# Kernel tuning notes

Hardware: AMD Instinct MI355X
Metric: run time of the kernel (lower is better)

The kernel has to match this reference:

```python
import jax, jax.numpy as jnp
import numpy as np

DIM = 768
HEADS = 6
HD = DIM // HEADS
B, N = 8, 4096
EPS = 1e-12  # torch F.normalize default


def setup_inputs() -> dict:
    key = jax.random.key(0)
    k1, k2, k3, k4, k5 = jax.random.split(key, 5)
    x = jax.random.normal(k1, (B, N, DIM), dtype=jnp.float32)
    y = jax.random.normal(k2, (B, N, DIM), dtype=jnp.float32)
    W_qkv = jax.random.normal(k3, (DIM, 2 * DIM), dtype=jnp.float32) * (1.0 / np.sqrt(DIM))
    temperature = jnp.ones((HEADS, 1, 1), dtype=jnp.float32)
    W_proj = jax.random.normal(k4, (DIM, DIM), dtype=jnp.float32) * (1.0 / np.sqrt(DIM))
    b_proj = jax.random.normal(k5, (DIM,), dtype=jnp.float32) * 0.01
    return {"x": x, "y": y, "W_qkv": W_qkv, "temperature": temperature,
            "W_proj": W_proj, "b_proj": b_proj}


def _l2norm(t):
    # F.normalize(dim=-1): v / max(||v||, eps)
    n = jnp.sqrt(jnp.sum(t * t, axis=-1, keepdims=True))
    return t / jnp.maximum(n, EPS)


def reference(x, y, W_qkv, temperature, W_proj, b_proj):
    Bx, Nx, C = x.shape
    # qkv: [B,N,2C] -> [B,N,2,H,hd] -> q,k: [B,H,hd,N]
    qkv = (x @ W_qkv).reshape(Bx, Nx, 2, HEADS, HD)
    qkv = jnp.transpose(qkv, (2, 0, 3, 4, 1))  # [2,B,H,hd,N]
    q, k = qkv[0], qkv[1]
    # v: [B,H,hd,N]
    v = jnp.transpose(y.reshape(Bx, Nx, HEADS, HD), (0, 2, 3, 1))
    q = _l2norm(q)  # normalize over token dim N
    k = _l2norm(k)
    # channel-channel attention: [B,H,hd,hd]
    attn = jnp.einsum('bhcn,bhdn->bhcd', q, k) * temperature
    attn = jax.nn.softmax(attn, axis=-1)
    out = jnp.einsum('bhcd,bhdn->bhcn', attn, v)  # [B,H,hd,N]
    out = jnp.transpose(out, (0, 3, 1, 2)).reshape(Bx, Nx, C)
    return out @ W_proj + b_proj
```

## Files before the change

kernel.cpp:

```cpp
#include <hip/hip_runtime.h>
#include <hip/hip_bf16.h>

using bf16 = __hip_bfloat16;
typedef __attribute__((ext_vector_type(4))) float f32x4;
typedef __attribute__((ext_vector_type(8))) short bf16x8;

constexpr int Ntok   = 4096;
constexpr int Cdim   = 768;
constexpr int Hn     = 6;
constexpr int HD     = 128;
constexpr int QKcols = 1536;

#define AS1 __attribute__((address_space(1)))
#define AS3 __attribute__((address_space(3)))

__device__ inline void gload_lds16(const bf16* g, bf16* l) {
    __builtin_amdgcn_global_load_lds((const AS1 void*)g, (AS3 void*)l, 16, 0, 0);
}

__device__ inline int4 cvt8_f32_to_bf16(const float* p) {
    const float4 a0 = *reinterpret_cast<const float4*>(p);
    const float4 a1 = *reinterpret_cast<const float4*>(p + 4);
    union { int4 i; bf16 h[8]; } u;
    u.h[0] = __float2bfloat16(a0.x); u.h[1] = __float2bfloat16(a0.y);
    u.h[2] = __float2bfloat16(a0.z); u.h[3] = __float2bfloat16(a0.w);
    u.h[4] = __float2bfloat16(a1.x); u.h[5] = __float2bfloat16(a1.y);
    u.h[6] = __float2bfloat16(a1.z); u.h[7] = __float2bfloat16(a1.w);
    return u.i;
}

__global__ __launch_bounds__(256) void cvt_kernel(const float* __restrict__ in,
                                                  bf16* __restrict__ out) {
    const size_t i = ((size_t)blockIdx.x * 256 + threadIdx.x) * 8;
    *reinterpret_cast<int4*>(out + i) = cvt8_f32_to_bf16(in + i);
}

__global__ void transpose_kernel(const float* __restrict__ W, bf16* __restrict__ Wt,
                                 int K, int N) {
    __shared__ bf16 tile[32][33];
    const int n0 = blockIdx.x * 32, k0 = blockIdx.y * 32;
    const int tx = threadIdx.x, ty = threadIdx.y;
    for (int i = 0; i < 32; i += 8)
        tile[ty + i][tx] = __float2bfloat16(W[(size_t)(k0 + ty + i) * N + n0 + tx]);
    __syncthreads();
    for (int i = 0; i < 32; i += 8)
        Wt[(size_t)(n0 + ty + i) * K + k0 + tx] = tile[tx][ty + i];
}

template <bool C_F32, bool BIAS>
__global__ __launch_bounds__(256) void gemm_bt(const bf16* __restrict__ A,
                                               const bf16* __restrict__ Bt,
                                               const float* __restrict__ bias,
                                               void* __restrict__ Cv,
                                               int M, int N, int K) {
    __shared__ bf16 As[128 * 32];
    __shared__ bf16 Bs[128 * 32];

    const int m0   = blockIdx.y * 128, n0 = blockIdx.x * 128;
    const int tid  = threadIdx.x;
    const int wave = tid >> 6, lane = tid & 63;
    const int wq   = wave >> 1, wr = wave & 1;
    const int lm   = lane & 15, quad = lane >> 4;

    const int srow = tid >> 2, scol = (tid & 3) * 8;
    const bf16* Ag = A  + (size_t)(m0 + srow) * K + scol;
    const bf16* Bg = Bt + (size_t)(n0 + srow) * K + scol;
    bf16* Al0 = &As[srow * 32 + scol];
    bf16* Al1 = &As[(64 + srow) * 32 + scol];
    bf16* Bl0 = &Bs[srow * 32 + scol];
    bf16* Bl1 = &Bs[(64 + srow) * 32 + scol];

    f32x4 acc[4][4] = {};

    for (int k0 = 0; k0 < K; k0 += 32) {
        __syncthreads();
        gload_lds16(Ag + k0,                Al0);
        gload_lds16(Ag + (size_t)64 * K + k0, Al1);
        gload_lds16(Bg + k0,                Bl0);
        gload_lds16(Bg + (size_t)64 * K + k0, Bl1);
        __syncthreads();

        bf16x8 af[4], bfr[4];
#pragma unroll
        for (int t = 0; t < 4; t++) {
            af[t]  = *reinterpret_cast<const bf16x8*>(&As[(wq * 64 + t * 16 + lm) * 32 + quad * 8]);
            bfr[t] = *reinterpret_cast<const bf16x8*>(&Bs[(wr * 64 + t * 16 + lm) * 32 + quad * 8]);
        }
#pragma unroll
        for (int mt = 0; mt < 4; mt++)
#pragma unroll
            for (int nt = 0; nt < 4; nt++)
                acc[mt][nt] = __builtin_amdgcn_mfma_f32_16x16x32_bf16(af[mt], bfr[nt], acc[mt][nt], 0, 0, 0);
    }

    const int cm = m0 + wq * 64, cn = n0 + wr * 64;
#pragma unroll
    for (int mt = 0; mt < 4; mt++) {
#pragma unroll
        for (int nt = 0; nt < 4; nt++) {
            const int col = cn + nt * 16 + lm;
            const float bv = BIAS ? bias[col] : 0.0f;
#pragma unroll
            for (int r = 0; r < 4; r++) {
                const int row = cm + mt * 16 + quad * 4 + r;
                if constexpr (C_F32)
                    ((float*)Cv)[(size_t)row * N + col] = acc[mt][nt][r] + bv;
                else
                    ((bf16*)Cv)[(size_t)row * N + col] = __float2bfloat16(acc[mt][nt][r] + bv);
            }
        }
    }
}

__global__ __launch_bounds__(256) void colnorm_kernel(const bf16* __restrict__ qkv,
                                                      float* __restrict__ invn) {
    const int b = blockIdx.y, j0 = blockIdx.x * 64;
    const int cg = threadIdx.x & 7;
    const int rg = threadIdx.x >> 3;
    const bf16* p = qkv + (size_t)b * Ntok * QKcols + (size_t)rg * 128 * QKcols + j0 + cg * 8;
    float s[8] = {};
    for (int r = 0; r < 128; r++) {
        bf16 h[8];
        *reinterpret_cast<int4*>(h) = *reinterpret_cast<const int4*>(p + (size_t)r * QKcols);
#pragma unroll
        for (int t = 0; t < 8; t++) { const float v = (float)h[t]; s[t] += v * v; }
    }
    __shared__ float red[256][8];
#pragma unroll
    for (int t = 0; t < 8; t++) red[threadIdx.x][t] = s[t];
    __syncthreads();
    if (threadIdx.x < 64) {
        const int cg2 = threadIdx.x >> 3, t2 = threadIdx.x & 7;
        float tot = 0.0f;
#pragma unroll
        for (int g = 0; g < 32; g++) tot += red[g * 8 + cg2][t2];
        invn[b * QKcols + j0 + threadIdx.x] = 1.0f / fmaxf(sqrtf(tot), 1e-12f);
    }
}

__global__ __launch_bounds__(256) void gram_partial_kernel(const bf16* __restrict__ qkv,
                                                           float* __restrict__ partial) {
    constexpr int BKn = 64;
    constexpr int LDT = BKn + 8;
    __shared__ bf16 Qt[HD * LDT];
    __shared__ bf16 Kt[HD * LDT];

    const int bh = blockIdx.x, nc = blockIdx.y, b = bh / Hn, h = bh % Hn;
    const int tid = threadIdx.x, wave = tid >> 6, lane = tid & 63;
    const int lm = lane & 15, quad = lane >> 4;
    const size_t base = (size_t)b * Ntok * QKcols;
    const int qoff = h * HD, koff = Cdim + h * HD;

    f32x4 acc[2][8] = {};

    for (int i = 0; i < 8; i++) {
        const int n0 = nc * 512 + i * BKn;
        __syncthreads();
#pragma unroll
        for (int r = 0; r < 4; r++) {
            const int chunk = tid + 256 * r;
            const int nl = chunk & 63;
            const int j0 = (chunk >> 6) * 8;
            bf16 vq[8], vk[8];
            *reinterpret_cast<int4*>(vq) = *reinterpret_cast<const int4*>(qkv + base + (size_t)(n0 + nl) * QKcols + qoff + j0);
            *reinterpret_cast<int4*>(vk) = *reinterpret_cast<const int4*>(qkv + base + (size_t)(n0 + nl) * QKcols + koff + j0);
#pragma unroll
            for (int t = 0; t < 8; t++) {
                Qt[(j0 + t) * LDT + nl] = vq[t];
                Kt[(j0 + t) * LDT + nl] = vk[t];
            }
        }
        __syncthreads();
#pragma unroll
        for (int ks = 0; ks < 2; ks++) {
            bf16x8 aq[2], bk[8];
#pragma unroll
            for (int mt = 0; mt < 2; mt++)
                aq[mt] = *reinterpret_cast<const bf16x8*>(&Qt[(wave * 32 + mt * 16 + lm) * LDT + ks * 32 + quad * 8]);
#pragma unroll
            for (int dt = 0; dt < 8; dt++)
                bk[dt] = *reinterpret_cast<const bf16x8*>(&Kt[(dt * 16 + lm) * LDT + ks * 32 + quad * 8]);
#pragma unroll
            for (int mt = 0; mt < 2; mt++)
#pragma unroll
                for (int dt = 0; dt < 8; dt++)
                    acc[mt][dt] = __builtin_amdgcn_mfma_f32_16x16x32_bf16(aq[mt], bk[dt], acc[mt][dt], 0, 0, 0);
        }
    }

    float* pp = partial + ((size_t)(bh * 8 + nc) * HD) * HD;
#pragma unroll
    for (int mt = 0; mt < 2; mt++)
#pragma unroll
        for (int dt = 0; dt < 8; dt++)
#pragma unroll
            for (int r = 0; r < 4; r++) {
                const int c = wave * 32 + mt * 16 + quad * 4 + r;
                pp[(size_t)c * HD + dt * 16 + lm] = acc[mt][dt][r];
            }
}

__global__ __launch_bounds__(256) void gram_reduce_softmax(const float* __restrict__ partial,
                                                           const float* __restrict__ invn,
                                                           const float* __restrict__ temp,
                                                           bf16* __restrict__ attn) {
    const int bh = blockIdx.x, b = bh / Hn, h = bh % Hn;
    const int r = threadIdx.x >> 1, hf = threadIdx.x & 1;
    const float th = temp[h];
    const float* invq = invn + b * QKcols + h * HD;
    const float* invk = invn + b * QKcols + Cdim + h * HD;

    float v[64];
    const float* pbase = partial + ((size_t)bh * 8 * HD + r) * HD + hf * 64;
#pragma unroll
    for (int t = 0; t < 64; t += 4)
        *reinterpret_cast<float4*>(&v[t]) = *reinterpret_cast<const float4*>(&pbase[t]);
    for (int p = 1; p < 8; p++) {
        const float* pp = pbase + (size_t)p * HD * HD;
#pragma unroll
        for (int t = 0; t < 64; t += 4) {
            const float4 u = *reinterpret_cast<const float4*>(&pp[t]);
            v[t] += u.x; v[t + 1] += u.y; v[t + 2] += u.z; v[t + 3] += u.w;
        }
    }
    const float iq = invq[r] * th;
    float mx = -1e30f;
#pragma unroll
    for (int t = 0; t < 64; t++) { v[t] *= iq * invk[hf * 64 + t]; mx = fmaxf(mx, v[t]); }
    mx = fmaxf(mx, __shfl_xor(mx, 1, 64));
    float sum = 0.0f;
#pragma unroll
    for (int t = 0; t < 64; t++) { v[t] = __expf(v[t] - mx); sum += v[t]; }
    sum += __shfl_xor(sum, 1, 64);
    const float inv = 1.0f / sum;
    bf16* orow = attn + ((size_t)bh * HD + r) * HD + hf * 64;
#pragma unroll
    for (int t = 0; t < 64; t++) orow[t] = __float2bfloat16(v[t] * inv);
}

__global__ __launch_bounds__(256) void pv_kernel(const bf16* __restrict__ attn,
                                                 const float* __restrict__ y,
                                                 bf16* __restrict__ out_pre) {
    constexpr int LDA = HD + 8;
    __shared__ bf16 Pw[HD * LDA];

    const int bh = blockIdx.y, b = bh / Hn, h = bh % Hn;
    const int nbase = blockIdx.x * 512;
    const int tid = threadIdx.x, wave = tid >> 6, lane = tid & 63;
    const int lm = lane & 15, quad = lane >> 4;

    const bf16* ap = attn + (size_t)bh * HD * HD;
#pragma unroll
    for (int r = 0; r < 8; r++) {
        const int chunk = tid + 256 * r;
        const int c = chunk >> 4, d0 = (chunk & 15) * 8;
        *reinterpret_cast<int4*>(&Pw[c * LDA + d0]) =
            *reinterpret_cast<const int4*>(ap + (size_t)c * HD + d0);
    }
    __syncthreads();

    const float* yh = y + (size_t)b * Ntok * Cdim + h * HD;
    for (int mt = 0; mt < 8; mt++) {
        const int nrow0 = nbase + wave * 128 + mt * 16;
        f32x4 acc[8] = {};
#pragma unroll
        for (int ks = 0; ks < 4; ks++) {
            const int4 ai = cvt8_f32_to_bf16(yh + (size_t)(nrow0 + lm) * Cdim + ks * 32 + quad * 8);
            const bf16x8 afr = *reinterpret_cast<const bf16x8*>(&ai);
#pragma unroll
            for (int ct = 0; ct < 8; ct++) {
                const bf16x8 bfr = *reinterpret_cast<const bf16x8*>(&Pw[(ct * 16 + lm) * LDA + ks * 32 + quad * 8]);
                acc[ct] = __builtin_amdgcn_mfma_f32_16x16x32_bf16(afr, bfr, acc[ct], 0, 0, 0);
            }
        }
        bf16* op = out_pre + (size_t)(b * Ntok + nrow0) * Cdim + h * HD;
#pragma unroll
        for (int ct = 0; ct < 8; ct++) {
            const int ccol = ct * 16 + lm;
#pragma unroll
            for (int r = 0; r < 4; r++)
                op[(size_t)(quad * 4 + r) * Cdim + ccol] = __float2bfloat16(acc[ct][r]);
        }
    }
}

extern "C" void kernel_launch(void* const* d_in, const int* in_sizes, int n_in,
                              void* d_out, int out_size, void* d_ws, size_t ws_size,
                              hipStream_t stream) {
    const float* x     = (const float*)d_in[0];
    const float* y     = (const float*)d_in[1];
    const float* Wqkv  = (const float*)d_in[2];
    const float* temp  = (const float*)d_in[3];
    const float* Wproj = (const float*)d_in[4];
    const float* bproj = (const float*)d_in[5];
    float* out = (float*)d_out;

    char* ws = (char*)d_ws;
    size_t o = 0;
    bf16* qkv     = (bf16*)(ws + o); o += (size_t)32768 * 1536 * 2;
    bf16* xb      = (bf16*)(ws + o);
    float* partial = (float*)xb;      o += (size_t)48 * 8 * 128 * 128 * 4;
    o = (o < (size_t)32768 * 1536 * 2 + (size_t)32768 * 768 * 2)
            ? (size_t)32768 * 1536 * 2 + (size_t)32768 * 768 * 2 : o;
    bf16* out_pre = (bf16*)(ws + o); o += (size_t)32768 * 768 * 2;
    bf16* Wt_qkv  = (bf16*)(ws + o); o += (size_t)1536 * 768 * 2;
    bf16* Wt_proj = (bf16*)(ws + o); o += (size_t)768 * 768 * 2;
    float* invn   = (float*)(ws + o); o += (size_t)8 * 1536 * 4;
    bf16* attnw   = (bf16*)(ws + o); o += (size_t)48 * 128 * 128 * 2;

    dim3 tb(32, 8);
    transpose_kernel<<<dim3(1536 / 32, 768 / 32), tb, 0, stream>>>(Wqkv, Wt_qkv, 768, 1536);
    transpose_kernel<<<dim3(768 / 32, 768 / 32), tb, 0, stream>>>(Wproj, Wt_proj, 768, 768);

    cvt_kernel<<<12288, 256, 0, stream>>>(x, xb);

    gemm_bt<false, false><<<dim3(1536 / 128, 32768 / 128), 256, 0, stream>>>(
        xb, Wt_qkv, nullptr, qkv, 32768, 1536, 768);

    colnorm_kernel<<<dim3(24, 8), 256, 0, stream>>>(qkv, invn);

    gram_partial_kernel<<<dim3(48, 8), 256, 0, stream>>>(qkv, partial);
    gram_reduce_softmax<<<48, 256, 0, stream>>>(partial, invn, temp, attnw);

    pv_kernel<<<dim3(8, 48), 256, 0, stream>>>(attnw, y, out_pre);

    gemm_bt<true, true><<<dim3(768 / 128, 32768 / 128), 256, 0, stream>>>(
        out_pre, Wt_proj, bproj, out, 32768, 768, 768);
}
```

Measured before the change: 523.7 us.

## Reassociate attention via per-batch Gram matrix and fused effective projection weight

```diff
diff --git a/kernel.cpp b/kernel.cpp
--- a/kernel.cpp
+++ b/kernel.cpp
@@ -52,11 +52,12 @@
                                                const bf16* __restrict__ Bt,
                                                const float* __restrict__ bias,
                                                void* __restrict__ Cv,
-                                               int M, int N, int K) {
+                                               int M, int N, int K, int bt_bstride) {
     __shared__ bf16 As[128 * 32];
     __shared__ bf16 Bs[128 * 32];
 
     const int m0   = blockIdx.y * 128, n0 = blockIdx.x * 128;
+    Bt += (size_t)(m0 >> 12) * bt_bstride;
     const int tid  = threadIdx.x;
     const int wave = tid >> 6, lane = tid & 63;
     const int wq   = wave >> 1, wr = wave & 1;
@@ -74,9 +75,9 @@
 
     for (int k0 = 0; k0 < K; k0 += 32) {
         __syncthreads();
-        gload_lds16(Ag + k0,                Al0);
+        gload_lds16(Ag + k0,                  Al0);
         gload_lds16(Ag + (size_t)64 * K + k0, Al1);
-        gload_lds16(Bg + k0,                Bl0);
+        gload_lds16(Bg + k0,                  Bl0);
         gload_lds16(Bg + (size_t)64 * K + k0, Bl1);
         __syncthreads();
 
@@ -112,49 +113,26 @@
     }
 }
 
-__global__ __launch_bounds__(256) void colnorm_kernel(const bf16* __restrict__ qkv,
-                                                      float* __restrict__ invn) {
-    const int b = blockIdx.y, j0 = blockIdx.x * 64;
-    const int cg = threadIdx.x & 7;
-    const int rg = threadIdx.x >> 3;
-    const bf16* p = qkv + (size_t)b * Ntok * QKcols + (size_t)rg * 128 * QKcols + j0 + cg * 8;
-    float s[8] = {};
-    for (int r = 0; r < 128; r++) {
-        bf16 h[8];
-        *reinterpret_cast<int4*>(h) = *reinterpret_cast<const int4*>(p + (size_t)r * QKcols);
-#pragma unroll
-        for (int t = 0; t < 8; t++) { const float v = (float)h[t]; s[t] += v * v; }
-    }
-    __shared__ float red[256][8];
-#pragma unroll
-    for (int t = 0; t < 8; t++) red[threadIdx.x][t] = s[t];
-    __syncthreads();
-    if (threadIdx.x < 64) {
-        const int cg2 = threadIdx.x >> 3, t2 = threadIdx.x & 7;
-        float tot = 0.0f;
-#pragma unroll
-        for (int g = 0; g < 32; g++) tot += red[g * 8 + cg2][t2];
-        invn[b * QKcols + j0 + threadIdx.x] = 1.0f / fmaxf(sqrtf(tot), 1e-12f);
-    }
-}
-
-__global__ __launch_bounds__(256) void gram_partial_kernel(const bf16* __restrict__ qkv,
-                                                           float* __restrict__ partial) {
+__global__ __launch_bounds__(256) void gram_x_kernel(const bf16* __restrict__ xb,
+                                                     bf16* __restrict__ G) {
     constexpr int BKn = 64;
     constexpr int LDT = BKn + 8;
     __shared__ bf16 Qt[HD * LDT];
     __shared__ bf16 Kt[HD * LDT];
 
-    const int bh = blockIdx.x, nc = blockIdx.y, b = bh / Hn, h = bh % Hn;
+    int ci = 0, rem = blockIdx.x, rowlen = 6;
+    while (rem >= rowlen) { rem -= rowlen; rowlen--; ci++; }
+    const int di = ci + rem;
+    const int b = blockIdx.y;
+    const int c0 = ci * 128, d0 = di * 128;
+
     const int tid = threadIdx.x, wave = tid >> 6, lane = tid & 63;
     const int lm = lane & 15, quad = lane >> 4;
-    const size_t base = (size_t)b * Ntok * QKcols;
-    const int qoff = h * HD, koff = Cdim + h * HD;
+    const size_t base = (size_t)b * Ntok * Cdim;
 
     f32x4 acc[2][8] = {};
 
-    for (int i = 0; i < 8; i++) {
-        const int n0 = nc * 512 + i * BKn;
+    for (int n0 = 0; n0 < Ntok; n0 += BKn) {
         __syncthreads();
 #pragma unroll
         for (int r = 0; r < 4; r++) {
@@ -162,12 +140,12 @@
             const int nl = chunk & 63;
             const int j0 = (chunk >> 6) * 8;
             bf16 vq[8], vk[8];
-            *reinterpret_cast<int4*>(vq) = *reinterpret_cast<const int4*>(qkv + base + (size_t)(n0 + nl) * QKcols + qoff + j0);
-            *reinterpret_cast<int4*>(vk) = *reinterpret_cast<const int4*>(qkv + base + (size_t)(n0 + nl) * QKcols + koff + j0);
-#pragma unroll
-            for (int t = 0; t < 8; t++) {
-                Qt[(j0 + t) * LDT + nl] = vq[t];
-                Kt[(j0 + t) * LDT + nl] = vk[t];
+            *reinterpret_cast<int4*>(vq) = *reinterpret_cast<const int4*>(xb + base + (size_t)(n0 + nl) * Cdim + c0 + j0);
+            *reinterpret_cast<int4*>(vk) = *reinterpret_cast<const int4*>(xb + base + (size_t)(n0 + nl) * Cdim + d0 + j0);
+#pragma unroll
+            for (int u = 0; u < 8; u++) {
+                Qt[(j0 + u) * LDT + nl] = vq[u];
+                Kt[(j0 + u) * LDT + nl] = vk[u];
             }
         }
         __syncthreads();
@@ -188,7 +166,7 @@
         }
     }
 
-    float* pp = partial + ((size_t)(bh * 8 + nc) * HD) * HD;
+    bf16* Gb = G + (size_t)b * Cdim * Cdim;
 #pragma unroll
     for (int mt = 0; mt < 2; mt++)
 #pragma unroll
@@ -196,91 +174,139 @@
 #pragma unroll
             for (int r = 0; r < 4; r++) {
                 const int c = wave * 32 + mt * 16 + quad * 4 + r;
-                pp[(size_t)c * HD + dt * 16 + lm] = acc[mt][dt][r];
+                const int d = dt * 16 + lm;
+                const bf16 v = __float2bfloat16(acc[mt][dt][r]);
+                Gb[(size_t)(c0 + c) * Cdim + d0 + d] = v;
+                if (ci != di) Gb[(size_t)(d0 + d) * Cdim + c0 + c] = v;
             }
 }
 
-__global__ __launch_bounds__(256) void gram_reduce_softmax(const float* __restrict__ partial,
-                                                           const float* __restrict__ invn,
-                                                           const float* __restrict__ temp,
-                                                           bf16* __restrict__ attn) {
+__global__ __launch_bounds__(256) void head_kernel(const bf16* __restrict__ GW,
+                                                   const bf16* __restrict__ Wtq,
+                                                   const bf16* __restrict__ Wtp,
+                                                   const float* __restrict__ temp,
+                                                   bf16* __restrict__ WeffT) {
+    constexpr int LDT = 72;
+    constexpr int LDP = 136;
+    __shared__ bf16 Kt[HD * LDT];
+    __shared__ bf16 At[HD * LDP];
+    __shared__ float invq[HD], invk[HD];
+
     const int bh = blockIdx.x, b = bh / Hn, h = bh % Hn;
-    const int r = threadIdx.x >> 1, hf = threadIdx.x & 1;
-    const float th = temp[h];
-    const float* invq = invn + b * QKcols + h * HD;
-    const float* invk = invn + b * QKcols + Cdim + h * HD;
-
-    float v[64];
-    const float* pbase = partial + ((size_t)bh * 8 * HD + r) * HD + hf * 64;
-#pragma unroll
-    for (int t = 0; t < 64; t += 4)
-        *reinterpret_cast<float4*>(&v[t]) = *reinterpret_cast<const float4*>(&pbase[t]);
-    for (int p = 1; p < 8; p++) {
-        const float* pp = pbase + (size_t)p * HD * HD;
-#pragma unroll
-        for (int t = 0; t < 64; t += 4) {
-            const float4 u = *reinterpret_cast<const float4*>(&pp[t]);
-            v[t] += u.x; v[t + 1] += u.y; v[t + 2] += u.z; v[t + 3] += u.w;
-        }
-    }
-    const float iq = invq[r] * th;
-    float mx = -1e30f;
-#pragma unroll
-    for (int t = 0; t < 64; t++) { v[t] *= iq * invk[hf * 64 + t]; mx = fmaxf(mx, v[t]); }
-    mx = fmaxf(mx, __shfl_xor(mx, 1, 64));
-    float sum = 0.0f;
-#pragma unroll
-    for (int t = 0; t < 64; t++) { v[t] = __expf(v[t] - mx); sum += v[t]; }
-    sum += __shfl_xor(sum, 1, 64);
-    const float inv = 1.0f / sum;
-    bf16* orow = attn + ((size_t)bh * HD + r) * HD + hf * 64;
-#pragma unroll
-    for (int t = 0; t < 64; t++) orow[t] = __float2bfloat16(v[t] * inv);
-}
-
-__global__ __launch_bounds__(256) void pv_kernel(const bf16* __restrict__ attn,
-                                                 const float* __restrict__ y,
-                                                 bf16* __restrict__ out_pre) {
-    constexpr int LDA = HD + 8;
-    __shared__ bf16 Pw[HD * LDA];
-
-    const int bh = blockIdx.y, b = bh / Hn, h = bh % Hn;
-    const int nbase = blockIdx.x * 512;
     const int tid = threadIdx.x, wave = tid >> 6, lane = tid & 63;
     const int lm = lane & 15, quad = lane >> 4;
-
-    const bf16* ap = attn + (size_t)bh * HD * HD;
-#pragma unroll
-    for (int r = 0; r < 8; r++) {
-        const int chunk = tid + 256 * r;
-        const int c = chunk >> 4, d0 = (chunk & 15) * 8;
-        *reinterpret_cast<int4*>(&Pw[c * LDA + d0]) =
-            *reinterpret_cast<const int4*>(ap + (size_t)c * HD + d0);
-    }
+    const int qoff = h * HD, koff = Cdim + h * HD;
+    const float th = temp[h];
+
+    {
+        const int cl = tid & 127;
+        const bool isk = tid >= 128;
+        const int colg = (isk ? koff : qoff) + cl;
+        const bf16* wt = Wtq + (size_t)colg * Cdim;
+        const bf16* gw = GW + (size_t)b * Cdim * QKcols + colg;
+        float s = 0.0f;
+        for (int r = 0; r < Cdim; r += 8) {
+            bf16 wv[8];
+            *reinterpret_cast<int4*>(wv) = *reinterpret_cast<const int4*>(wt + r);
+#pragma unroll
+            for (int u = 0; u < 8; u++)
+                s += (float)wv[u] * (float)gw[(size_t)(r + u) * QKcols];
+        }
+        (isk ? invk : invq)[cl] = 1.0f / fmaxf(sqrtf(fmaxf(s, 0.0f)), 1e-12f);
+    }
+
+    f32x4 acc[2][8] = {};
+    const bf16* GWk = GW + (size_t)b * Cdim * QKcols + koff;
+    for (int r0 = 0; r0 < Cdim; r0 += 64) {
+        __syncthreads();
+#pragma unroll
+        for (int rr = 0; rr < 4; rr++) {
+            const int chunk = tid + 256 * rr;
+            const int rl = chunk & 63;
+            const int j0 = (chunk >> 6) * 8;
+            bf16 vk[8];
+            *reinterpret_cast<int4*>(vk) = *reinterpret_cast<const int4*>(GWk + (size_t)(r0 + rl) * QKcols + j0);
+#pragma unroll
+            for (int u = 0; u < 8; u++)
+                Kt[(j0 + u) * LDT + rl] = vk[u];
+        }
+        __syncthreads();
+#pragma unroll
+        for (int ks = 0; ks < 2; ks++) {
+            bf16x8 aq[2], bk[8];
+#pragma unroll
+            for (int mt = 0; mt < 2; mt++)
+                aq[mt] = *reinterpret_cast<const bf16x8*>(Wtq + (size_t)(qoff + wave * 32 + mt * 16 + lm) * Cdim + r0 + ks * 32 + quad * 8);
+#pragma unroll
+            for (int dt = 0; dt < 8; dt++)
+                bk[dt] = *reinterpret_cast<const bf16x8*>(&Kt[(dt * 16 + lm) * LDT + ks * 32 + quad * 8]);
+#pragma unroll
+            for (int mt = 0; mt < 2; mt++)
+#pragma unroll
+                for (int dt = 0; dt < 8; dt++)
+                    acc[mt][dt] = __builtin_amdgcn_mfma_f32_16x16x32_bf16(aq[mt], bk[dt], acc[mt][dt], 0, 0, 0);
+        }
+    }
+
     __syncthreads();
-
-    const float* yh = y + (size_t)b * Ntok * Cdim + h * HD;
-    for (int mt = 0; mt < 8; mt++) {
-        const int nrow0 = nbase + wave * 128 + mt * 16;
-        f32x4 acc[8] = {};
+    float ikv[8];
+#pragma unroll
+    for (int dt = 0; dt < 8; dt++) ikv[dt] = invk[dt * 16 + lm] * th;
+#pragma unroll
+    for (int mt = 0; mt < 2; mt++) {
+#pragma unroll
+        for (int r = 0; r < 4; r++) {
+            const int c = wave * 32 + mt * 16 + quad * 4 + r;
+            const float iq = invq[c];
+            float v[8], m = -1e30f;
+#pragma unroll
+            for (int dt = 0; dt < 8; dt++) { v[dt] = acc[mt][dt][r] * iq * ikv[dt]; m = fmaxf(m, v[dt]); }
+            m = fmaxf(m, __shfl_xor(m, 1, 64));
+            m = fmaxf(m, __shfl_xor(m, 2, 64));
+            m = fmaxf(m, __shfl_xor(m, 4, 64));
+            m = fmaxf(m, __shfl_xor(m, 8, 64));
+            float sum = 0.0f;
+#pragma unroll
+            for (int dt = 0; dt < 8; dt++) { v[dt] = __expf(v[dt] - m); sum += v[dt]; }
+            sum += __shfl_xor(sum, 1, 64);
+            sum += __shfl_xor(sum, 2, 64);
+            sum += __shfl_xor(sum, 4, 64);
+            sum += __shfl_xor(sum, 8, 64);
+            const float inv = 1.0f / sum;
+#pragma unroll
+            for (int dt = 0; dt < 8; dt++)
+                At[(dt * 16 + lm) * LDP + c] = __float2bfloat16(v[dt] * inv);
+        }
+    }
+    __syncthreads();
+
+    bf16* Wo = WeffT + (size_t)b * Cdim * Cdim + h * HD;
+    for (int jo = 0; jo < Cdim; jo += 256) {
+        const int jb = jo + wave * 64;
+        f32x4 a2[4][8] = {};
 #pragma unroll
         for (int ks = 0; ks < 4; ks++) {
-            const int4 ai = cvt8_f32_to_bf16(yh + (size_t)(nrow0 + lm) * Cdim + ks * 32 + quad * 8);
-            const bf16x8 afr = *reinterpret_cast<const bf16x8*>(&ai);
-#pragma unroll
-            for (int ct = 0; ct < 8; ct++) {
-                const bf16x8 bfr = *reinterpret_cast<const bf16x8*>(&Pw[(ct * 16 + lm) * LDA + ks * 32 + quad * 8]);
-                acc[ct] = __builtin_amdgcn_mfma_f32_16x16x32_bf16(afr, bfr, acc[ct], 0, 0, 0);
-            }
-        }
-        bf16* op = out_pre + (size_t)(b * Ntok + nrow0) * Cdim + h * HD;
-#pragma unroll
-        for (int ct = 0; ct < 8; ct++) {
-            const int ccol = ct * 16 + lm;
-#pragma unroll
-            for (int r = 0; r < 4; r++)
-                op[(size_t)(quad * 4 + r) * Cdim + ccol] = __float2bfloat16(acc[ct][r]);
-        }
+            bf16x8 aw[4], bp[8];
+#pragma unroll
+            for (int mt = 0; mt < 4; mt++)
+                aw[mt] = *reinterpret_cast<const bf16x8*>(Wtp + (size_t)(jb + mt * 16 + lm) * Cdim + h * HD + ks * 32 + quad * 8);
+#pragma unroll
+            for (int dt = 0; dt < 8; dt++)
+                bp[dt] = *reinterpret_cast<const bf16x8*>(&At[(dt * 16 + lm) * LDP + ks * 32 + quad * 8]);
+#pragma unroll
+            for (int mt = 0; mt < 4; mt++)
+#pragma unroll
+                for (int dt = 0; dt < 8; dt++)
+                    a2[mt][dt] = __builtin_amdgcn_mfma_f32_16x16x32_bf16(aw[mt], bp[dt], a2[mt][dt], 0, 0, 0);
+        }
+#pragma unroll
+        for (int mt = 0; mt < 4; mt++)
+#pragma unroll
+            for (int dt = 0; dt < 8; dt++)
+#pragma unroll
+                for (int r = 0; r < 4; r++)
+                    Wo[(size_t)(jb + mt * 16 + quad * 4 + r) * Cdim + dt * 16 + lm] =
+                        __float2bfloat16(a2[mt][dt][r]);
     }
 }
 
@@ -297,33 +323,28 @@
 
     char* ws = (char*)d_ws;
     size_t o = 0;
-    bf16* qkv     = (bf16*)(ws + o); o += (size_t)32768 * 1536 * 2;
-    bf16* xb      = (bf16*)(ws + o);
-    float* partial = (float*)xb;      o += (size_t)48 * 8 * 128 * 128 * 4;
-    o = (o < (size_t)32768 * 1536 * 2 + (size_t)32768 * 768 * 2)
-            ? (size_t)32768 * 1536 * 2 + (size_t)32768 * 768 * 2 : o;
-    bf16* out_pre = (bf16*)(ws + o); o += (size_t)32768 * 768 * 2;
+    bf16* xb      = (bf16*)(ws + o); o += (size_t)32768 * 768 * 2;
+    bf16* yb      = (bf16*)(ws + o); o += (size_t)32768 * 768 * 2;
+    bf16* G       = (bf16*)(ws + o); o += (size_t)8 * 768 * 768 * 2;
+    bf16* GW      = (bf16*)(ws + o); o += (size_t)8 * 768 * 1536 * 2;
+    bf16* WeffT   = (bf16*)(ws + o); o += (size_t)8 * 768 * 768 * 2;
     bf16* Wt_qkv  = (bf16*)(ws + o); o += (size_t)1536 * 768 * 2;
     bf16* Wt_proj = (bf16*)(ws + o); o += (size_t)768 * 768 * 2;
-    float* invn   = (float*)(ws + o); o += (size_t)8 * 1536 * 4;
-    bf16* attnw   = (bf16*)(ws + o); o += (size_t)48 * 128 * 128 * 2;
 
     dim3 tb(32, 8);
     transpose_kernel<<<dim3(1536 / 32, 768 / 32), tb, 0, stream>>>(Wqkv, Wt_qkv, 768, 1536);
     transpose_kernel<<<dim3(768 / 32, 768 / 32), tb, 0, stream>>>(Wproj, Wt_proj, 768, 768);
 
     cvt_kernel<<<12288, 256, 0, stream>>>(x, xb);
-
-    gemm_bt<false, false><<<dim3(1536 / 128, 32768 / 128), 256, 0, stream>>>(
-        xb, Wt_qkv, nullptr, qkv, 32768, 1536, 768);
-
-    colnorm_kernel<<<dim3(24, 8), 256, 0, stream>>>(qkv, invn);
-
-    gram_partial_kernel<<<dim3(48, 8), 256, 0, stream>>>(qkv, partial);
-    gram_reduce_softmax<<<48, 256, 0, stream>>>(partial, invn, temp, attnw);
-
-    pv_kernel<<<dim3(8, 48), 256, 0, stream>>>(attnw, y, out_pre);
+    cvt_kernel<<<12288, 256, 0, stream>>>(y, yb);
+
+    gram_x_kernel<<<dim3(21, 8), 256, 0, stream>>>(xb, G);
+
+    gemm_bt<false, false><<<dim3(1536 / 128, 6144 / 128), 256, 0, stream>>>(
+        G, Wt_qkv, nullptr, GW, 6144, 1536, 768, 0);
+
+    head_kernel<<<48, 256, 0, stream>>>(GW, Wt_qkv, Wt_proj, temp, WeffT);
 
     gemm_bt<true, true><<<dim3(768 / 128, 32768 / 128), 256, 0, stream>>>(
-        out_pre, Wt_proj, bproj, out, 32768, 768, 768);
-}
+        yb, WeffT, bproj, out, 32768, 768, 768, 768 * 768);
+}
```

Measured after the change: 566.6 us. +8.2%, slower.
